# Performance work log

Measured on AMD Instinct MI355X. Metric: run time of the kernel, lower is better.

Reference implementation:

```python
import jax, jax.numpy as jnp
import numpy as np

N_NODES = 100000
N_EDGES = 1200000
IN_DIM = 64
OUT_DIM = 64


def setup_inputs() -> dict:
    key = jax.random.key(0)
    k1, k2, k3 = jax.random.split(key, 3)
    x = jax.random.normal(k1, (N_NODES, IN_DIM), dtype=jnp.float32)
    edge_index = jax.random.randint(k2, (2, N_EDGES), 0, N_NODES, dtype=jnp.int32)
    W = jax.random.normal(k3, (IN_DIM, OUT_DIM), dtype=jnp.float32) * (1.0 / np.sqrt(IN_DIM))
    b = jnp.zeros((OUT_DIM,), dtype=jnp.float32)
    return {"x": x, "edge_index": edge_index, "W": W, "b": b}


def reference(x, edge_index, W, b):
    # GCN layer: out = D^{-1/2} A D^{-1/2} X W + b, A given as edge list.
    src, dst = edge_index[0], edge_index[1]
    ones = jnp.ones((src.shape[0],), dtype=x.dtype)
    deg_out = jax.ops.segment_sum(ones, src, num_segments=N_NODES)  # [N]
    deg_in = jax.ops.segment_sum(ones, dst, num_segments=N_NODES)   # [N]
    deg_out = jnp.maximum(deg_out, 1.0)
    deg_in = jnp.maximum(deg_in, 1.0)
    # per-edge symmetric normalization coefficient
    norm = jax.lax.rsqrt(deg_out[src] * deg_in[dst])  # [E]
    msgs = x[src] * norm[:, None]                      # [E, IN_DIM] gather
    agg = jax.ops.segment_sum(msgs, dst, num_segments=N_NODES)  # [N, IN_DIM] scatter-add
    return agg @ W + b                                 # [N, OUT_DIM]
```

## Files before the change

### kernel.cpp

```cpp
#include <hip/hip_runtime.h>

#define N_NODES 100000
#define N_EDGES 1200000
#define DIM 64
#define RB 13
#define RSZ 8192
#define SC 8
#define NBIN (RB * SC)
#define CAPB 13312
#define ACH 512
#define A_GRID 3910
#define N_SCAN_BLOCKS ((N_NODES + 255) / 256)

__global__ __launch_bounds__(256) void phaseA(
    const int* __restrict__ src, const int* __restrict__ dst,
    const float* __restrict__ x, const float* __restrict__ W,
    int* __restrict__ curD, int* __restrict__ curS,
    uint2* __restrict__ binD, int* __restrict__ binS,
    unsigned short* __restrict__ yb) {
  __shared__ float Ws[64][64];
  __shared__ float xs[64][64];
  __shared__ int cntD[RB], cntS[RB], bD[RB], bS[RB];
  int blk = blockIdx.x;
  int m5 = blk % 5;

  if (m5 >= 3) {
    int g = (blk / 5) * 2 + (m5 - 3);
    int row0 = g * 64;
    if (row0 >= N_NODES) return;

    const float4* W4 = (const float4*)W;
    float4* Ws4 = (float4*)&Ws[0][0];
    for (int i = threadIdx.x; i < 64 * 16; i += 256) Ws4[i] = W4[i];

    int nrows = N_NODES - row0;
    if (nrows > 64) nrows = 64;
    const float4* x4 = (const float4*)(x + (size_t)row0 * DIM);
    float4* xs4 = (float4*)&xs[0][0];
    for (int i = threadIdx.x; i < nrows * 16; i += 256) xs4[i] = x4[i];
    __syncthreads();

    int col = threadIdx.x & 63;
    int rg = threadIdx.x >> 6;
    float acc[16];
#pragma unroll
    for (int j = 0; j < 16; ++j) acc[j] = 0.f;
    for (int k = 0; k < 64; ++k) {
      float w = Ws[k][col];
#pragma unroll
      for (int j = 0; j < 16; ++j) acc[j] += xs[rg + 4 * j][k] * w;
    }
#pragma unroll
    for (int j = 0; j < 16; ++j) {
      int r = rg + 4 * j;
      if (r < nrows) {
        unsigned int bits = __float_as_uint(acc[j]);
        unsigned int rb = (bits + 0x7fffu + ((bits >> 16) & 1u)) >> 16;
        yb[(size_t)(row0 + r) * DIM + col] = (unsigned short)rb;
      }
    }
  } else {
    int f = (blk / 5) * 3 + m5;
    int c = f & (SC - 1);
    int e0 = f * ACH;
    if (threadIdx.x < RB) {
      cntD[threadIdx.x] = 0;
      cntS[threadIdx.x] = 0;
    }
    __syncthreads();
    int sv[2], dv[2], rd[2], rs[2], kd[2], ks[2];
    bool ok[2];
#pragma unroll
    for (int j = 0; j < 2; ++j) {
      int e = e0 + threadIdx.x + j * 256;
      ok[j] = e < N_EDGES;
      if (ok[j]) {
        sv[j] = src[e];
        dv[j] = dst[e];
        rd[j] = dv[j] >> 13;
        rs[j] = sv[j] >> 13;
        kd[j] = atomicAdd(&cntD[rd[j]], 1);
        ks[j] = atomicAdd(&cntS[rs[j]], 1);
      }
    }
    __syncthreads();
    if (threadIdx.x < RB) {
      bD[threadIdx.x] = atomicAdd(&curD[threadIdx.x * SC + c], cntD[threadIdx.x]);
      bS[threadIdx.x] = atomicAdd(&curS[threadIdx.x * SC + c], cntS[threadIdx.x]);
    }
    __syncthreads();
#pragma unroll
    for (int j = 0; j < 2; ++j) {
      if (ok[j]) {
        int p = bD[rd[j]] + kd[j];
        if (p < CAPB) {
          uint2 pr;
          pr.x = (unsigned)dv[j];
          pr.y = (unsigned)sv[j];
          binD[(size_t)(rd[j] * SC + c) * CAPB + p] = pr;
        }
        int q = bS[rs[j]] + ks[j];
        if (q < CAPB) binS[(size_t)(rs[j] * SC + c) * CAPB + q] = sv[j];
      }
    }
  }
}

__global__ __launch_bounds__(1024) void k1_hist(
    const int* __restrict__ curD, const int* __restrict__ curS,
    const uint2* __restrict__ binD, const int* __restrict__ binS,
    int* __restrict__ PI, int* __restrict__ deg_out) {
  __shared__ int h[RSZ];
  int tid = threadIdx.x;
  int b = blockIdx.x;
  for (int i = tid; i < RSZ; i += 1024) h[i] = 0;
  __syncthreads();

  if (b < NBIN) {
    int n0 = (b >> 3) << 13;
    int cnt = curD[b];
    if (cnt > CAPB) cnt = CAPB;
    const uint2* bp = binD + (size_t)b * CAPB;
    for (int i = tid; i < cnt; i += 1024) atomicAdd(&h[(int)bp[i].x - n0], 1);
    __syncthreads();
    int* pb = PI + (size_t)b * RSZ;
    for (int i = tid; i < RSZ; i += 1024) pb[i] = h[i];
  } else {
    int bb = b - NBIN;
    int n0 = (bb >> 3) << 13;
    int cnt = curS[bb];
    if (cnt > CAPB) cnt = CAPB;
    const int* bp = binS + (size_t)bb * CAPB;
    for (int i = tid; i < cnt; i += 1024) atomicAdd(&h[bp[i] - n0], 1);
    __syncthreads();
    for (int i = tid; i < RSZ; i += 1024) {
      int n = n0 + i;
      if (n < N_NODES && h[i]) atomicAdd(&deg_out[n], h[i]);
    }
  }
}

__global__ __launch_bounds__(256) void reduce_pi(
    int* __restrict__ PI, int* __restrict__ deg_in) {
  int i = blockIdx.x * 256 + threadIdx.x;
  if (i >= RB * RSZ) return;
  int r = i >> 13;
  int off = i & (RSZ - 1);
  int sI = 0;
#pragma unroll
  for (int c = 0; c < SC; ++c) {
    size_t idx = (size_t)(r * SC + c) * RSZ + off;
    int t = PI[idx];
    PI[idx] = sI;
    sI += t;
  }
  if (i < N_NODES) deg_in[i] = sI;
}

__global__ __launch_bounds__(256) void scan1(
    const int* __restrict__ deg_in, int* __restrict__ row_ptr,
    int* __restrict__ blocksums) {
  int i = blockIdx.x * 256 + threadIdx.x;
  int v = (i < N_NODES) ? deg_in[i] : 0;
  int lane = threadIdx.x & 63;
  int wid = threadIdx.x >> 6;
  int incl = v;
#pragma unroll
  for (int off = 1; off < 64; off <<= 1) {
    int n = __shfl_up(incl, off, 64);
    if (lane >= off) incl += n;
  }
  __shared__ int wsum[4];
  if (lane == 63) wsum[wid] = incl;
  __syncthreads();
  int wofs = 0;
  for (int w = 0; w < wid; ++w) wofs += wsum[w];
  if (i < N_NODES) row_ptr[i] = wofs + incl - v;
  if (threadIdx.x == 0)
    blocksums[blockIdx.x] = wsum[0] + wsum[1] + wsum[2] + wsum[3];
}

__global__ __launch_bounds__(512) void scan2(int* __restrict__ blocksums) {
  int i = threadIdx.x;
  int v = (i < N_SCAN_BLOCKS) ? blocksums[i] : 0;
  int lane = i & 63;
  int wid = i >> 6;
  int incl = v;
#pragma unroll
  for (int off = 1; off < 64; off <<= 1) {
    int n = __shfl_up(incl, off, 64);
    if (lane >= off) incl += n;
  }
  __shared__ int wsum[8];
  if (lane == 63) wsum[wid] = incl;
  __syncthreads();
  int wofs = 0;
  for (int w = 0; w < wid; ++w) wofs += wsum[w];
  if (i < N_SCAN_BLOCKS) blocksums[i] = wofs + incl - v;
}

__global__ __launch_bounds__(256) void scan3(
    int* __restrict__ row_ptr, const int* __restrict__ blocksums) {
  int i = blockIdx.x * 256 + threadIdx.x;
  if (i < N_NODES) row_ptr[i] += blocksums[blockIdx.x];
}

__global__ __launch_bounds__(1024) void k2_fill_scale(
    const int* __restrict__ curD, const uint2* __restrict__ binD,
    const int* __restrict__ PI, const int* __restrict__ row_ptr,
    const int* __restrict__ deg_out, int* __restrict__ csr_src,
    unsigned short* __restrict__ yb) {
  __shared__ int base[RSZ];
  int tid = threadIdx.x;
  int b = blockIdx.x;

  if (b < NBIN) {
    int n0 = (b >> 3) << 13;
    int cnt = curD[b];
    if (cnt > CAPB) cnt = CAPB;
    const int* pb = PI + (size_t)b * RSZ;
    for (int i = tid; i < RSZ; i += 1024) {
      int n = n0 + i;
      base[i] = (n < N_NODES) ? row_ptr[n] + pb[i] : 0;
    }
    __syncthreads();
    const uint2* bp = binD + (size_t)b * CAPB;
    for (int i = tid; i < cnt; i += 1024) {
      uint2 p = bp[i];
      int pos = atomicAdd(&base[(int)p.x - n0], 1);
      csr_src[pos] = (int)p.y;
    }
  } else {
    int t = (b - NBIN) * 1024 + tid;
    if (t >= N_NODES * (DIM / 8)) return;
    int n = t >> 3;
    float rs = rsqrtf(fmaxf((float)deg_out[n], 1.f));
    uint4* p = (uint4*)yb + t;
    uint4 v = *p;
#pragma unroll
    for (int j = 0; j < 4; ++j) {
      unsigned int u = (&v.x)[j];
      float lo = __uint_as_float(u << 16) * rs;
      float hi = __uint_as_float(u & 0xffff0000u) * rs;
      unsigned int bl = __float_as_uint(lo);
      bl = (bl + 0x7fffu + ((bl >> 16) & 1u)) >> 16;
      unsigned int bh = __float_as_uint(hi);
      bh = (bh + 0x7fffu + ((bh >> 16) & 1u)) & 0xffff0000u;
      (&v.x)[j] = bl | bh;
    }
    *p = v;
  }
}

__global__ __launch_bounds__(256) void gather_y4(
    const int* __restrict__ row_ptr, const int* __restrict__ deg_in,
    const int* __restrict__ csr_src, const unsigned short* __restrict__ yb,
    const float* __restrict__ b, float* __restrict__ out) {
  int wv = threadIdx.x >> 6;
  int lane = threadIdx.x & 63;
  int n = blockIdx.x * 4 + wv;
  if (n >= N_NODES) return;
  int degi = deg_in[n];
  int deg = degi < 64 ? degi : 64;
  int beg = row_ptr[n];
  int sv = (lane < deg) ? csr_src[beg + lane] : 0;

  int eg = lane >> 3;
  int c = lane & 7;

  float acc[8];
#pragma unroll
  for (int j = 0; j < 8; ++j) acc[j] = 0.f;

  for (int e = 0; e < deg; e += 8) {
    int idx = e + eg;
    int s = __shfl(sv, idx);
    if (idx < deg) {
      uint4 v = *(const uint4*)(yb + ((size_t)s << 6) + (c << 3));
#pragma unroll
      for (int j = 0; j < 4; ++j) {
        unsigned int u = (&v.x)[j];
        acc[2 * j] += __uint_as_float(u << 16);
        acc[2 * j + 1] += __uint_as_float(u & 0xffff0000u);
      }
    }
  }

#pragma unroll
  for (int off = 8; off < 64; off <<= 1) {
#pragma unroll
    for (int j = 0; j < 8; ++j) acc[j] += __shfl_xor(acc[j], off);
  }

  if (lane < 8) {
    float rs_in = rsqrtf(fmaxf((float)degi, 1.f));
    const float4* b4 = (const float4*)b;
    float4 ba = b4[2 * c], bb = b4[2 * c + 1];
    float4 o0, o1;
    o0.x = acc[0] * rs_in + ba.x;
    o0.y = acc[1] * rs_in + ba.y;
    o0.z = acc[2] * rs_in + ba.z;
    o0.w = acc[3] * rs_in + ba.w;
    o1.x = acc[4] * rs_in + bb.x;
    o1.y = acc[5] * rs_in + bb.y;
    o1.z = acc[6] * rs_in + bb.z;
    o1.w = acc[7] * rs_in + bb.w;
    float4* o4 = (float4*)(out + (size_t)n * DIM + (c << 3));
    o4[0] = o0;
    o4[1] = o1;
  }
}

extern "C" void kernel_launch(void* const* d_in, const int* in_sizes, int n_in,
                              void* d_out, int out_size, void* d_ws, size_t ws_size,
                              hipStream_t stream) {
  const float* x = (const float*)d_in[0];
  const int* edge_index = (const int*)d_in[1];
  const float* W = (const float*)d_in[2];
  const float* b = (const float*)d_in[3];
  float* out = (float*)d_out;

  const int* src = edge_index;
  const int* dst = edge_index + N_EDGES;

  uint2* binD = (uint2*)d_ws;
  int* binS = (int*)(binD + (size_t)NBIN * CAPB);
  int* csr_src = binS;
  int* PI = binS + (size_t)NBIN * CAPB;
  int* row_ptr = PI + (size_t)NBIN * RSZ;
  int* deg_in = row_ptr + N_NODES;
  int* deg_out = deg_in + N_NODES;
  int* blocksums = deg_out + N_NODES;
  int* cur = blocksums + 512;
  int* curD = cur;
  int* curS = cur + 128;
  unsigned short* yb = (unsigned short*)(cur + 256);

  hipMemsetAsync(deg_out, 0, (size_t)(N_NODES + 512 + 256) * sizeof(int), stream);

  phaseA<<<A_GRID, 256, 0, stream>>>(src, dst, x, W, curD, curS, binD, binS, yb);

  k1_hist<<<2 * NBIN, 1024, 0, stream>>>(curD, curS, binD, binS, PI, deg_out);

  reduce_pi<<<(RB * RSZ + 255) / 256, 256, 0, stream>>>(PI, deg_in);

  scan1<<<N_SCAN_BLOCKS, 256, 0, stream>>>(deg_in, row_ptr, blocksums);
  scan2<<<1, 512, 0, stream>>>(blocksums);
  scan3<<<N_SCAN_BLOCKS, 256, 0, stream>>>(row_ptr, blocksums);

  int scale_blocks = (N_NODES * (DIM / 8) + 1023) / 1024;
  k2_fill_scale<<<NBIN + scale_blocks, 1024, 0, stream>>>(
      curD, binD, PI, row_ptr, deg_out, csr_src, yb);

  gather_y4<<<(N_NODES + 3) / 4, 256, 0, stream>>>(row_ptr, deg_in, csr_src, yb,
                                                   b, out);
}
```

Baseline: 219.3 us.

## Pack edge bins compactly, fuse degree reduce with scan, drop scan3 launch

```diff
diff --git a/kernel.cpp b/kernel.cpp
--- a/kernel.cpp
+++ b/kernel.cpp
@@ -11,16 +11,19 @@
 #define ACH 512
 #define A_GRID 3910
 #define N_SCAN_BLOCKS ((N_NODES + 255) / 256)
+#define N_RS_BLOCKS ((RB * RSZ + 255) / 256)
 
 __global__ __launch_bounds__(256) void phaseA(
     const int* __restrict__ src, const int* __restrict__ dst,
     const float* __restrict__ x, const float* __restrict__ W,
     int* __restrict__ curD, int* __restrict__ curS,
-    uint2* __restrict__ binD, int* __restrict__ binS,
+    int* __restrict__ binD, unsigned short* __restrict__ binS,
     unsigned short* __restrict__ yb) {
   __shared__ float Ws[64][64];
   __shared__ float xs[64][64];
-  __shared__ int cntD[RB], cntS[RB], bD[RB], bS[RB];
+  __shared__ int cnt[2][8][16];
+  __shared__ int boff[2][8][16];
+  __shared__ int bBase[2][16];
   int blk = blockIdx.x;
   int m5 = blk % 5;
 
@@ -63,11 +66,11 @@
     int f = (blk / 5) * 3 + m5;
     int c = f & (SC - 1);
     int e0 = f * ACH;
-    if (threadIdx.x < RB) {
-      cntD[threadIdx.x] = 0;
-      cntS[threadIdx.x] = 0;
-    }
-    __syncthreads();
+    {
+      ((int*)cnt)[threadIdx.x] = 0;
+    }
+    __syncthreads();
+    int wid = threadIdx.x >> 6;
     int sv[2], dv[2], rd[2], rs[2], kd[2], ks[2];
     bool ok[2];
 #pragma unroll
@@ -75,32 +78,48 @@
       int e = e0 + threadIdx.x + j * 256;
       ok[j] = e < N_EDGES;
       if (ok[j]) {
+        int vw = wid * 2 + j;
         sv[j] = src[e];
         dv[j] = dst[e];
         rd[j] = dv[j] >> 13;
         rs[j] = sv[j] >> 13;
-        kd[j] = atomicAdd(&cntD[rd[j]], 1);
-        ks[j] = atomicAdd(&cntS[rs[j]], 1);
+        kd[j] = atomicAdd(&cnt[0][vw][rd[j]], 1);
+        ks[j] = atomicAdd(&cnt[1][vw][rs[j]], 1);
       }
     }
     __syncthreads();
     if (threadIdx.x < RB) {
-      bD[threadIdx.x] = atomicAdd(&curD[threadIdx.x * SC + c], cntD[threadIdx.x]);
-      bS[threadIdx.x] = atomicAdd(&curS[threadIdx.x * SC + c], cntS[threadIdx.x]);
+      int r = threadIdx.x;
+      int run = 0;
+#pragma unroll
+      for (int vw = 0; vw < 8; ++vw) {
+        boff[0][vw][r] = run;
+        run += cnt[0][vw][r];
+      }
+      bBase[0][r] = atomicAdd(&curD[r * SC + c], run);
+    } else if (threadIdx.x >= 16 && threadIdx.x < 16 + RB) {
+      int r = threadIdx.x - 16;
+      int run = 0;
+#pragma unroll
+      for (int vw = 0; vw < 8; ++vw) {
+        boff[1][vw][r] = run;
+        run += cnt[1][vw][r];
+      }
+      bBase[1][r] = atomicAdd(&curS[r * SC + c], run);
     }
     __syncthreads();
 #pragma unroll
     for (int j = 0; j < 2; ++j) {
       if (ok[j]) {
-        int p = bD[rd[j]] + kd[j];
-        if (p < CAPB) {
-          uint2 pr;
-          pr.x = (unsigned)dv[j];
-          pr.y = (unsigned)sv[j];
-          binD[(size_t)(rd[j] * SC + c) * CAPB + p] = pr;
-        }
-        int q = bS[rs[j]] + ks[j];
-        if (q < CAPB) binS[(size_t)(rs[j] * SC + c) * CAPB + q] = sv[j];
+        int vw = wid * 2 + j;
+        int p = bBase[0][rd[j]] + boff[0][vw][rd[j]] + kd[j];
+        if (p < CAPB)
+          binD[(size_t)(rd[j] * SC + c) * CAPB + p] =
+              (sv[j] << 13) | (dv[j] & (RSZ - 1));
+        int q = bBase[1][rs[j]] + boff[1][vw][rs[j]] + ks[j];
+        if (q < CAPB)
+          binS[(size_t)(rs[j] * SC + c) * CAPB + q] =
+              (unsigned short)(sv[j] & (RSZ - 1));
       }
     }
   }
@@ -108,7 +127,7 @@
 
 __global__ __launch_bounds__(1024) void k1_hist(
     const int* __restrict__ curD, const int* __restrict__ curS,
-    const uint2* __restrict__ binD, const int* __restrict__ binS,
+    const int* __restrict__ binD, const unsigned short* __restrict__ binS,
     int* __restrict__ PI, int* __restrict__ deg_out) {
   __shared__ int h[RSZ];
   int tid = threadIdx.x;
@@ -117,11 +136,11 @@
   __syncthreads();
 
   if (b < NBIN) {
-    int n0 = (b >> 3) << 13;
     int cnt = curD[b];
     if (cnt > CAPB) cnt = CAPB;
-    const uint2* bp = binD + (size_t)b * CAPB;
-    for (int i = tid; i < cnt; i += 1024) atomicAdd(&h[(int)bp[i].x - n0], 1);
+    const int* bp = binD + (size_t)b * CAPB;
+    for (int i = tid; i < cnt; i += 1024)
+      atomicAdd(&h[bp[i] & (RSZ - 1)], 1);
     __syncthreads();
     int* pb = PI + (size_t)b * RSZ;
     for (int i = tid; i < RSZ; i += 1024) pb[i] = h[i];
@@ -130,8 +149,8 @@
     int n0 = (bb >> 3) << 13;
     int cnt = curS[bb];
     if (cnt > CAPB) cnt = CAPB;
-    const int* bp = binS + (size_t)bb * CAPB;
-    for (int i = tid; i < cnt; i += 1024) atomicAdd(&h[bp[i] - n0], 1);
+    const unsigned short* bp = binS + (size_t)bb * CAPB;
+    for (int i = tid; i < cnt; i += 1024) atomicAdd(&h[bp[i]], 1);
     __syncthreads();
     for (int i = tid; i < RSZ; i += 1024) {
       int n = n0 + i;
@@ -140,35 +159,34 @@
   }
 }
 
-__global__ __launch_bounds__(256) void reduce_pi(
-    int* __restrict__ PI, int* __restrict__ deg_in) {
-  int i = blockIdx.x * 256 + threadIdx.x;
-  if (i >= RB * RSZ) return;
-  int r = i >> 13;
-  int off = i & (RSZ - 1);
-  int sI = 0;
-#pragma unroll
-  for (int c = 0; c < SC; ++c) {
-    size_t idx = (size_t)(r * SC + c) * RSZ + off;
-    int t = PI[idx];
-    PI[idx] = sI;
-    sI += t;
-  }
-  if (i < N_NODES) deg_in[i] = sI;
-}
-
-__global__ __launch_bounds__(256) void scan1(
-    const int* __restrict__ deg_in, int* __restrict__ row_ptr,
+__global__ __launch_bounds__(256) void reduce_scan(
+    int* __restrict__ PI, int* __restrict__ deg_in, int* __restrict__ row_ptr,
     int* __restrict__ blocksums) {
   int i = blockIdx.x * 256 + threadIdx.x;
-  int v = (i < N_NODES) ? deg_in[i] : 0;
+  int v = 0;
+  if (i < RB * RSZ) {
+    int r = i >> 13;
+    int off = i & (RSZ - 1);
+    int sI = 0;
+#pragma unroll
+    for (int c = 0; c < SC; ++c) {
+      size_t idx = (size_t)(r * SC + c) * RSZ + off;
+      int t = PI[idx];
+      PI[idx] = sI;
+      sI += t;
+    }
+    if (i < N_NODES) {
+      deg_in[i] = sI;
+      v = sI;
+    }
+  }
   int lane = threadIdx.x & 63;
   int wid = threadIdx.x >> 6;
   int incl = v;
 #pragma unroll
   for (int off = 1; off < 64; off <<= 1) {
-    int n = __shfl_up(incl, off, 64);
-    if (lane >= off) incl += n;
+    int u = __shfl_up(incl, off, 64);
+    if (lane >= off) incl += u;
   }
   __shared__ int wsum[4];
   if (lane == 63) wsum[wid] = incl;
@@ -199,17 +217,11 @@
   if (i < N_SCAN_BLOCKS) blocksums[i] = wofs + incl - v;
 }
 
-__global__ __launch_bounds__(256) void scan3(
-    int* __restrict__ row_ptr, const int* __restrict__ blocksums) {
-  int i = blockIdx.x * 256 + threadIdx.x;
-  if (i < N_NODES) row_ptr[i] += blocksums[blockIdx.x];
-}
-
 __global__ __launch_bounds__(1024) void k2_fill_scale(
-    const int* __restrict__ curD, const uint2* __restrict__ binD,
+    const int* __restrict__ curD, const int* __restrict__ binD,
     const int* __restrict__ PI, const int* __restrict__ row_ptr,
-    const int* __restrict__ deg_out, int* __restrict__ csr_src,
-    unsigned short* __restrict__ yb) {
+    const int* __restrict__ blocksums, const int* __restrict__ deg_out,
+    int* __restrict__ csr_src, unsigned short* __restrict__ yb) {
   __shared__ int base[RSZ];
   int tid = threadIdx.x;
   int b = blockIdx.x;
@@ -221,14 +233,14 @@
     const int* pb = PI + (size_t)b * RSZ;
     for (int i = tid; i < RSZ; i += 1024) {
       int n = n0 + i;
-      base[i] = (n < N_NODES) ? row_ptr[n] + pb[i] : 0;
-    }
-    __syncthreads();
-    const uint2* bp = binD + (size_t)b * CAPB;
+      base[i] = (n < N_NODES) ? row_ptr[n] + blocksums[n >> 8] + pb[i] : 0;
+    }
+    __syncthreads();
+    const int* bp = binD + (size_t)b * CAPB;
     for (int i = tid; i < cnt; i += 1024) {
-      uint2 p = bp[i];
-      int pos = atomicAdd(&base[(int)p.x - n0], 1);
-      csr_src[pos] = (int)p.y;
+      int v = bp[i];
+      int pos = atomicAdd(&base[v & (RSZ - 1)], 1);
+      csr_src[pos] = v >> 13;
     }
   } else {
     int t = (b - NBIN) * 1024 + tid;
@@ -253,16 +265,17 @@
 }
 
 __global__ __launch_bounds__(256) void gather_y4(
-    const int* __restrict__ row_ptr, const int* __restrict__ deg_in,
-    const int* __restrict__ csr_src, const unsigned short* __restrict__ yb,
-    const float* __restrict__ b, float* __restrict__ out) {
+    const int* __restrict__ row_ptr, const int* __restrict__ blocksums,
+    const int* __restrict__ deg_in, const int* __restrict__ csr_src,
+    const unsigned short* __restrict__ yb, const float* __restrict__ b,
+    float* __restrict__ out) {
   int wv = threadIdx.x >> 6;
   int lane = threadIdx.x & 63;
   int n = blockIdx.x * 4 + wv;
   if (n >= N_NODES) return;
   int degi = deg_in[n];
   int deg = degi < 64 ? degi : 64;
-  int beg = row_ptr[n];
+  int beg = row_ptr[n] + blocksums[n >> 8];
   int sv = (lane < deg) ? csr_src[beg + lane] : 0;
 
   int eg = lane >> 3;
@@ -323,10 +336,10 @@
   const int* src = edge_index;
   const int* dst = edge_index + N_EDGES;
 
-  uint2* binD = (uint2*)d_ws;
-  int* binS = (int*)(binD + (size_t)NBIN * CAPB);
-  int* csr_src = binS;
-  int* PI = binS + (size_t)NBIN * CAPB;
+  int* binD = (int*)d_ws;
+  unsigned short* binS = (unsigned short*)(binD + (size_t)NBIN * CAPB);
+  int* csr_src = (int*)(binS + (size_t)NBIN * CAPB);
+  int* PI = csr_src + N_EDGES;
   int* row_ptr = PI + (size_t)NBIN * RSZ;
   int* deg_in = row_ptr + N_NODES;
   int* deg_out = deg_in + N_NODES;
@@ -342,16 +355,13 @@
 
   k1_hist<<<2 * NBIN, 1024, 0, stream>>>(curD, curS, binD, binS, PI, deg_out);
 
-  reduce_pi<<<(RB * RSZ + 255) / 256, 256, 0, stream>>>(PI, deg_in);
-
-  scan1<<<N_SCAN_BLOCKS, 256, 0, stream>>>(deg_in, row_ptr, blocksums);
+  reduce_scan<<<N_RS_BLOCKS, 256, 0, stream>>>(PI, deg_in, row_ptr, blocksums);
   scan2<<<1, 512, 0, stream>>>(blocksums);
-  scan3<<<N_SCAN_BLOCKS, 256, 0, stream>>>(row_ptr, blocksums);
 
   int scale_blocks = (N_NODES * (DIM / 8) + 1023) / 1024;
   k2_fill_scale<<<NBIN + scale_blocks, 1024, 0, stream>>>(
-      curD, binD, PI, row_ptr, deg_out, csr_src, yb);
-
-  gather_y4<<<(N_NODES + 3) / 4, 256, 0, stream>>>(row_ptr, deg_in, csr_src, yb,
-                                                   b, out);
-}
+      curD, binD, PI, row_ptr, blocksums, deg_out, csr_src, yb);
+
+  gather_y4<<<(N_NODES + 3) / 4, 256, 0, stream>>>(row_ptr, blocksums, deg_in,
+                                                   csr_src, yb, b, out);
+}
```

New measurement: 209.9 us. 4.3% less time.
